# Performance work log

Measured on AMD Instinct MI355X. Metric: run time of the kernel, lower is better.

Reference implementation:

```python
import jax, jax.numpy as jnp
import numpy as np

D_MODEL = 1024
D_HIDDEN = 4096
NUM_BANKS = 16
NUM_SELECTED = 2


def setup_inputs() -> dict:
    key = jax.random.key(0)
    ks = jax.random.split(key, 7)
    s = 0.02
    return {
        "tensor": jax.random.normal(ks[0], (4, 1024, D_MODEL), dtype=jnp.float32),
        "Wr": jax.random.normal(ks[1], (D_MODEL, NUM_BANKS), dtype=jnp.float32) * s,
        "br": jnp.zeros((NUM_BANKS,), dtype=jnp.float32),
        "W1": jax.random.normal(ks[2], (NUM_BANKS, D_MODEL, D_HIDDEN), dtype=jnp.float32) * s,
        "b1": jnp.zeros((NUM_BANKS, D_HIDDEN), dtype=jnp.float32),
        "W2": jax.random.normal(ks[3], (NUM_BANKS, D_HIDDEN, D_MODEL), dtype=jnp.float32) * s,
        "b2": jnp.zeros((NUM_BANKS, D_MODEL), dtype=jnp.float32),
    }


def reference(tensor, Wr, br, W1, b1, W2, b2):
    # Router: softmax over banks, keep top-k probabilities (BankSelector)
    logits = jnp.einsum("bsd,de->bse", tensor, Wr) + br          # [B,S,E]
    probs = jax.nn.softmax(logits, axis=-1)
    topv, topi = jax.lax.top_k(probs, NUM_SELECTED)              # [B,S,K]
    # Dense gate [B,S,E]: selected banks carry their router probability,
    # all other banks are zeroed (equivalent to sparse dispatch/combine).
    gate = jnp.sum(jax.nn.one_hot(topi, NUM_BANKS, dtype=tensor.dtype)
                   * topv[..., None], axis=-2)                    # [B,S,E]
    # Banked expert FFN (BankedLinear x2 with ReLU between)
    h = jax.nn.relu(jnp.einsum("bsd,edh->bseh", tensor, W1) + b1)  # [B,S,E,Dh]
    y = jnp.einsum("bseh,ehm->bsem", h, W2) + b2                   # [B,S,E,Dm]
    # Weighted combine across selected banks
    out = jnp.einsum("bse,bsem->bsm", gate, y)                     # [B,S,Dm]
    return out
```

## Files before the change

kernel.cpp:

```cpp
#include <hip/hip_runtime.h>
#include <stdint.h>

#define D_MODEL   1024
#define D_HIDDEN  4096
#define NBANKS    16
#define NTOK      4096

#define BM 128
#define BN 128
#define BK 32
#define LDSK 56

typedef __attribute__((ext_vector_type(8))) short bf16x8;
typedef __attribute__((ext_vector_type(4))) float f32x4;

__device__ __forceinline__ unsigned short f2bf(float f) {
  unsigned u = __builtin_bit_cast(unsigned, f);
  u += 0x7FFFu + ((u >> 16) & 1u);
  return (unsigned short)(u >> 16);
}

__global__ __launch_bounds__(256) void zero_out_k(float4* __restrict__ out4,
                                                  int* __restrict__ counts) {
  size_t i = (size_t)blockIdx.x * 256 + threadIdx.x;
  out4[i] = make_float4(0.f, 0.f, 0.f, 0.f);
  if (blockIdx.x == 0 && threadIdx.x < NBANKS) counts[threadIdx.x] = 0;
}

__global__ __launch_bounds__(64) void router_k(const float* __restrict__ x,
                                               const float* __restrict__ Wr,
                                               const float* __restrict__ br,
                                               int* __restrict__ topIdx,
                                               float* __restrict__ topGate) {
  const int t = blockIdx.x;
  const int l = threadIdx.x;
  const float* xr = x + (size_t)t * D_MODEL;

  float acc[NBANKS];
#pragma unroll
  for (int e = 0; e < NBANKS; ++e) acc[e] = 0.f;

  for (int d = l; d < D_MODEL; d += 64) {
    const float xv = xr[d];
    const float* wrow = Wr + (size_t)d * NBANKS;
#pragma unroll
    for (int e = 0; e < NBANKS; ++e) acc[e] += xv * wrow[e];
  }
#pragma unroll
  for (int e = 0; e < NBANKS; ++e) {
#pragma unroll
    for (int m = 1; m < 64; m <<= 1) acc[e] += __shfl_xor(acc[e], m, 64);
  }
#pragma unroll
  for (int e = 0; e < NBANKS; ++e) acc[e] += br[e];

  if (l == 0) {
    float mx = acc[0];
#pragma unroll
    for (int e = 1; e < NBANKS; ++e) mx = fmaxf(mx, acc[e]);
    float p[NBANKS];
    float s = 0.f;
#pragma unroll
    for (int e = 0; e < NBANKS; ++e) { p[e] = expf(acc[e] - mx); s += p[e]; }
    int i0 = 0; float v0 = p[0];
#pragma unroll
    for (int e = 1; e < NBANKS; ++e) if (p[e] > v0) { v0 = p[e]; i0 = e; }
    int i1 = -1; float v1 = -1.f;
#pragma unroll
    for (int e = 0; e < NBANKS; ++e) if (e != i0 && p[e] > v1) { v1 = p[e]; i1 = e; }
    const float inv = 1.f / s;
    topIdx[2 * t]     = i0;
    topIdx[2 * t + 1] = i1;
    topGate[2 * t]     = v0 * inv;
    topGate[2 * t + 1] = v1 * inv;
  }
}

__global__ __launch_bounds__(256) void build_lists_k(const int* __restrict__ topIdx,
                                                     const float* __restrict__ topGate,
                                                     int* __restrict__ counts,
                                                     int* __restrict__ rowlist,
                                                     float* __restrict__ gatelist) {
  const int t = blockIdx.x * 256 + threadIdx.x;
  if (t >= NTOK) return;
#pragma unroll
  for (int k = 0; k < 2; ++k) {
    const int e = topIdx[2 * t + k];
    const int p = atomicAdd(&counts[e], 1);
    rowlist[e * NTOK + p]  = t;
    gatelist[e * NTOK + p] = topGate[2 * t + k];
  }
}

__global__ void scan_k(const int* __restrict__ counts, int* __restrict__ bankOff) {
  if (threadIdx.x == 0) {
    int s = 0;
#pragma unroll
    for (int e = 0; e < NBANKS; ++e) { bankOff[e] = s; s += counts[e]; }
    bankOff[NBANKS] = s;
  }
}

__global__ __launch_bounds__(256) void gemm1_k(const float* __restrict__ X,
                                               const float* __restrict__ W1,
                                               const float* __restrict__ b1,
                                               const int* __restrict__ counts,
                                               const int* __restrict__ bankOff,
                                               const int* __restrict__ rowlist,
                                               unsigned short* __restrict__ H) {
  const int e   = blockIdx.z;
  const int cnt = counts[e];
  const int m0  = blockIdx.y * BM;
  if (m0 >= cnt) return;
  const int n0  = blockIdx.x * BN;

  const int tid  = threadIdx.x;
  const int lane = tid & 63;
  const int w    = tid >> 6;
  const int wm   = (w >> 1) * 64;
  const int wn   = (w & 1) * 64;

  __shared__ unsigned short Xs[BM][LDSK];
  __shared__ unsigned short Ws[BN][LDSK];

  const int ar = tid >> 1;
  const int ak = (tid & 1) * 16;
  const int gi = min(m0 + ar, cnt - 1);
  const int tok = rowlist[e * NTOK + gi];
  const float* Arow = X + (size_t)tok * D_MODEL;

  const int bn = tid & 127;
  const int bg = tid >> 7;
  const float* Wb = W1 + (size_t)e * D_MODEL * D_HIDDEN;

  f32x4 acc[4][4];
#pragma unroll
  for (int i = 0; i < 4; ++i)
#pragma unroll
    for (int j = 0; j < 4; ++j)
#pragma unroll
      for (int r = 0; r < 4; ++r) acc[i][j][r] = 0.f;

  for (int k0 = 0; k0 < D_MODEL; k0 += BK) {
    {
      const float4* src = (const float4*)(Arow + k0 + ak);
      const float4 f0 = src[0], f1 = src[1], f2 = src[2], f3 = src[3];
      bf16x8 v0, v1;
      v0[0]=(short)f2bf(f0.x); v0[1]=(short)f2bf(f0.y); v0[2]=(short)f2bf(f0.z); v0[3]=(short)f2bf(f0.w);
      v0[4]=(short)f2bf(f1.x); v0[5]=(short)f2bf(f1.y); v0[6]=(short)f2bf(f1.z); v0[7]=(short)f2bf(f1.w);
      v1[0]=(short)f2bf(f2.x); v1[1]=(short)f2bf(f2.y); v1[2]=(short)f2bf(f2.z); v1[3]=(short)f2bf(f2.w);
      v1[4]=(short)f2bf(f3.x); v1[5]=(short)f2bf(f3.y); v1[6]=(short)f2bf(f3.z); v1[7]=(short)f2bf(f3.w);
      *((bf16x8*)&Xs[ar][ak])     = v0;
      *((bf16x8*)&Xs[ar][ak + 8]) = v1;
    }
#pragma unroll
    for (int i = 0; i < 4; ++i) {
      const int kb = bg * 4 + i * 8;
      const float* wp = Wb + (size_t)(k0 + kb) * D_HIDDEN + n0 + bn;
      const float a0 = wp[0];
      const float a1 = wp[D_HIDDEN];
      const float a2 = wp[2 * D_HIDDEN];
      const float a3 = wp[3 * D_HIDDEN];
      const unsigned long long pv =
          (unsigned long long)f2bf(a0)
        | ((unsigned long long)f2bf(a1) << 16)
        | ((unsigned long long)f2bf(a2) << 32)
        | ((unsigned long long)f2bf(a3) << 48);
      *((unsigned long long*)&Ws[bn][kb]) = pv;
    }
    __syncthreads();

    const int fr = lane & 15;
    const int fc = (lane >> 4) * 8;
    bf16x8 af[4], bfv[4];
#pragma unroll
    for (int mb = 0; mb < 4; ++mb) af[mb]  = *(const bf16x8*)&Xs[wm + mb * 16 + fr][fc];
#pragma unroll
    for (int nb = 0; nb < 4; ++nb) bfv[nb] = *(const bf16x8*)&Ws[wn + nb * 16 + fr][fc];
#pragma unroll
    for (int mb = 0; mb < 4; ++mb)
#pragma unroll
      for (int nb = 0; nb < 4; ++nb)
        acc[mb][nb] = __builtin_amdgcn_mfma_f32_16x16x32_bf16(af[mb], bfv[nb], acc[mb][nb], 0, 0, 0);
    __syncthreads();
  }

  const int hb = bankOff[e] + m0;
#pragma unroll
  for (int nb = 0; nb < 4; ++nb) {
    const int col = n0 + wn + nb * 16 + (lane & 15);
    const float bias = b1[e * D_HIDDEN + col];
#pragma unroll
    for (int mb = 0; mb < 4; ++mb)
#pragma unroll
      for (int r = 0; r < 4; ++r) {
        const int rowT = wm + mb * 16 + (lane >> 4) * 4 + r;
        if (m0 + rowT < cnt) {
          float v = acc[mb][nb][r] + bias;
          v = fmaxf(v, 0.f);
          H[(size_t)(hb + rowT) * D_HIDDEN + col] = f2bf(v);
        }
      }
  }
}

__global__ __launch_bounds__(256) void gemm2_k(const unsigned short* __restrict__ H,
                                               const float* __restrict__ W2,
                                               const float* __restrict__ b2,
                                               const int* __restrict__ counts,
                                               const int* __restrict__ bankOff,
                                               const int* __restrict__ rowlist,
                                               const float* __restrict__ gatelist,
                                               float* __restrict__ out) {
  const int e   = blockIdx.z;
  const int cnt = counts[e];
  const int m0  = blockIdx.y * BM;
  if (m0 >= cnt) return;
  const int n0  = blockIdx.x * BN;

  const int tid  = threadIdx.x;
  const int lane = tid & 63;
  const int w    = tid >> 6;
  const int wm   = (w >> 1) * 64;
  const int wn   = (w & 1) * 64;

  __shared__ unsigned short Xs[BM][LDSK];
  __shared__ unsigned short Ws[BN][LDSK];

  const int ar = tid >> 1;
  const int ak = (tid & 1) * 16;
  const int hb = bankOff[e];
  const int gi = hb + min(m0 + ar, cnt - 1);
  const unsigned short* Arow = H + (size_t)gi * D_HIDDEN;

  const int bn = tid & 127;
  const int bg = tid >> 7;
  const float* Wb = W2 + (size_t)e * D_HIDDEN * D_MODEL;

  f32x4 acc[4][4];
#pragma unroll
  for (int i = 0; i < 4; ++i)
#pragma unroll
    for (int j = 0; j < 4; ++j)
#pragma unroll
      for (int r = 0; r < 4; ++r) acc[i][j][r] = 0.f;

  for (int k0 = 0; k0 < D_HIDDEN; k0 += BK) {
    *((bf16x8*)&Xs[ar][ak])     = *(const bf16x8*)(Arow + k0 + ak);
    *((bf16x8*)&Xs[ar][ak + 8]) = *(const bf16x8*)(Arow + k0 + ak + 8);
#pragma unroll
    for (int i = 0; i < 4; ++i) {
      const int kb = bg * 4 + i * 8;
      const float* wp = Wb + (size_t)(k0 + kb) * D_MODEL + n0 + bn;
      const float a0 = wp[0];
      const float a1 = wp[D_MODEL];
      const float a2 = wp[2 * D_MODEL];
      const float a3 = wp[3 * D_MODEL];
      const unsigned long long pv =
          (unsigned long long)f2bf(a0)
        | ((unsigned long long)f2bf(a1) << 16)
        | ((unsigned long long)f2bf(a2) << 32)
        | ((unsigned long long)f2bf(a3) << 48);
      *((unsigned long long*)&Ws[bn][kb]) = pv;
    }
    __syncthreads();

    const int fr = lane & 15;
    const int fc = (lane >> 4) * 8;
    bf16x8 af[4], bfv[4];
#pragma unroll
    for (int mb = 0; mb < 4; ++mb) af[mb]  = *(const bf16x8*)&Xs[wm + mb * 16 + fr][fc];
#pragma unroll
    for (int nb = 0; nb < 4; ++nb) bfv[nb] = *(const bf16x8*)&Ws[wn + nb * 16 + fr][fc];
#pragma unroll
    for (int mb = 0; mb < 4; ++mb)
#pragma unroll
      for (int nb = 0; nb < 4; ++nb)
        acc[mb][nb] = __builtin_amdgcn_mfma_f32_16x16x32_bf16(af[mb], bfv[nb], acc[mb][nb], 0, 0, 0);
    __syncthreads();
  }

  float bias[4];
#pragma unroll
  for (int nb = 0; nb < 4; ++nb)
    bias[nb] = b2[e * D_MODEL + n0 + wn + nb * 16 + (lane & 15)];

#pragma unroll
  for (int mb = 0; mb < 4; ++mb)
#pragma unroll
    for (int r = 0; r < 4; ++r) {
      const int rowT = wm + mb * 16 + (lane >> 4) * 4 + r;
      if (m0 + rowT < cnt) {
        const int sidx = e * NTOK + m0 + rowT;
        const int tok  = rowlist[sidx];
        const float g  = gatelist[sidx];
        float* orow = out + (size_t)tok * D_MODEL;
#pragma unroll
        for (int nb = 0; nb < 4; ++nb) {
          const int col = n0 + wn + nb * 16 + (lane & 15);
          atomicAdd(&orow[col], g * (acc[mb][nb][r] + bias[nb]));
        }
      }
    }
}

extern "C" void kernel_launch(void* const* d_in, const int* in_sizes, int n_in,
                              void* d_out, int out_size, void* d_ws, size_t ws_size,
                              hipStream_t stream) {
  const float* X  = (const float*)d_in[0];
  const float* Wr = (const float*)d_in[1];
  const float* br = (const float*)d_in[2];
  const float* W1 = (const float*)d_in[3];
  const float* b1 = (const float*)d_in[4];
  const float* W2 = (const float*)d_in[5];
  const float* b2 = (const float*)d_in[6];
  float* out = (float*)d_out;

  char* w = (char*)d_ws;
  int*   topIdx   = (int*)(w);
  float* topGate  = (float*)(w + (32 << 10));
  int*   counts   = (int*)(w + (64 << 10));
  int*   bankOff  = (int*)(w + (64 << 10) + 256);
  int*   rowlist  = (int*)(w + (66 << 10));
  float* gatelist = (float*)(w + (66 << 10) + NBANKS * NTOK * 4);
  unsigned short* H = (unsigned short*)(w + (1 << 20));

  const size_t needed = (size_t)(1 << 20) + (size_t)(NTOK * 2) * D_HIDDEN * 2;
  if (ws_size < needed) return;

  zero_out_k<<<dim3(4096), dim3(256), 0, stream>>>((float4*)out, counts);
  router_k<<<dim3(NTOK), dim3(64), 0, stream>>>(X, Wr, br, topIdx, topGate);
  build_lists_k<<<dim3(16), dim3(256), 0, stream>>>(topIdx, topGate, counts, rowlist, gatelist);
  scan_k<<<dim3(1), dim3(64), 0, stream>>>(counts, bankOff);
  gemm1_k<<<dim3(D_HIDDEN / BN, NTOK / BM, NBANKS), dim3(256), 0, stream>>>(
      X, W1, b1, counts, bankOff, rowlist, H);
  gemm2_k<<<dim3(D_MODEL / BN, NTOK / BM, NBANKS), dim3(256), 0, stream>>>(
      H, W2, b2, counts, bankOff, rowlist, gatelist, out);
}
```

Measured before the change: 498.9 us.

## Swizzle LDS tiles, vectorize weight loads and use packed bf16 conversion

Replaces padded LDS arrays with an XOR-swizzled unpadded layout to avoid bank conflicts. Weight tile loads become float4 reads covering a 4x4 block per thread, transposed in registers, instead of scalar strided loads. FP32-to-bf16 conversion uses the packed v_cvt_pk_bf16_f32 instruction instead of manual rounding. LDS fragment addresses are precomputed outside the K loop. This reduces global load instruction count and ALU conversion overhead, but the swizzle pattern must avoid new conflicts on the 8-byte weight stores.

```diff
diff --git a/kernel.cpp b/kernel.cpp
--- a/kernel.cpp
+++ b/kernel.cpp
@@ -9,15 +9,27 @@
 #define BM 128
 #define BN 128
 #define BK 32
-#define LDSK 56
 
 typedef __attribute__((ext_vector_type(8))) short bf16x8;
 typedef __attribute__((ext_vector_type(4))) float f32x4;
+typedef __attribute__((ext_vector_type(4))) unsigned int u32x4;
+typedef __attribute__((ext_vector_type(2))) unsigned int u32x2;
 
 __device__ __forceinline__ unsigned short f2bf(float f) {
   unsigned u = __builtin_bit_cast(unsigned, f);
   u += 0x7FFFu + ((u >> 16) & 1u);
   return (unsigned short)(u >> 16);
+}
+
+__device__ __forceinline__ unsigned cvtpk(float lo, float hi) {
+  unsigned r;
+  asm("v_cvt_pk_bf16_f32 %0, %1, %2" : "=v"(r) : "v"(lo), "v"(hi));
+  return r;
+}
+
+__device__ __forceinline__ int swz(int row, int col) {
+  const int c = (col >> 3) ^ ((row >> 1) & 3);
+  return row * 32 + c * 8 + (col & 7);
 }
 
 __global__ __launch_bounds__(256) void zero_out_k(float4* __restrict__ out4,
@@ -120,18 +132,34 @@
   const int wm   = (w >> 1) * 64;
   const int wn   = (w & 1) * 64;
 
-  __shared__ unsigned short Xs[BM][LDSK];
-  __shared__ unsigned short Ws[BN][LDSK];
+  __shared__ unsigned short Xs[BM * BK];
+  __shared__ unsigned short Ws[BN * BK];
 
   const int ar = tid >> 1;
   const int ak = (tid & 1) * 16;
   const int gi = min(m0 + ar, cnt - 1);
   const int tok = rowlist[e * NTOK + gi];
-  const float* Arow = X + (size_t)tok * D_MODEL;
-
-  const int bn = tid & 127;
-  const int bg = tid >> 7;
-  const float* Wb = W1 + (size_t)e * D_MODEL * D_HIDDEN;
+  const float* Asrc = X + (size_t)tok * D_MODEL + ak;
+  unsigned short* xsw0 = &Xs[swz(ar, ak)];
+  unsigned short* xsw1 = &Xs[swz(ar, ak + 8)];
+
+  const int bn4 = (tid & 31) * 4;
+  const int bk4 = (tid >> 5) * 4;
+  const float* Bsrc = W1 + (size_t)e * D_MODEL * D_HIDDEN + (size_t)bk4 * D_HIDDEN + n0 + bn4;
+  unsigned short* wsw0 = &Ws[swz(bn4 + 0, bk4)];
+  unsigned short* wsw1 = &Ws[swz(bn4 + 1, bk4)];
+  unsigned short* wsw2 = &Ws[swz(bn4 + 2, bk4)];
+  unsigned short* wsw3 = &Ws[swz(bn4 + 3, bk4)];
+
+  const int fr = lane & 15;
+  const int fc = (lane >> 4) * 8;
+  const unsigned short* arp[4];
+  const unsigned short* brp[4];
+#pragma unroll
+  for (int i = 0; i < 4; ++i) {
+    arp[i] = &Xs[swz(wm + i * 16 + fr, fc)];
+    brp[i] = &Ws[swz(wn + i * 16 + fr, fc)];
+  }
 
   f32x4 acc[4][4];
 #pragma unroll
@@ -143,40 +171,39 @@
 
   for (int k0 = 0; k0 < D_MODEL; k0 += BK) {
     {
-      const float4* src = (const float4*)(Arow + k0 + ak);
-      const float4 f0 = src[0], f1 = src[1], f2 = src[2], f3 = src[3];
-      bf16x8 v0, v1;
-      v0[0]=(short)f2bf(f0.x); v0[1]=(short)f2bf(f0.y); v0[2]=(short)f2bf(f0.z); v0[3]=(short)f2bf(f0.w);
-      v0[4]=(short)f2bf(f1.x); v0[5]=(short)f2bf(f1.y); v0[6]=(short)f2bf(f1.z); v0[7]=(short)f2bf(f1.w);
-      v1[0]=(short)f2bf(f2.x); v1[1]=(short)f2bf(f2.y); v1[2]=(short)f2bf(f2.z); v1[3]=(short)f2bf(f2.w);
-      v1[4]=(short)f2bf(f3.x); v1[5]=(short)f2bf(f3.y); v1[6]=(short)f2bf(f3.z); v1[7]=(short)f2bf(f3.w);
-      *((bf16x8*)&Xs[ar][ak])     = v0;
-      *((bf16x8*)&Xs[ar][ak + 8]) = v1;
+      const float4* s4 = (const float4*)(Asrc + k0);
+      const float4 f0 = s4[0], f1 = s4[1], f2 = s4[2], f3 = s4[3];
+      u32x4 v0, v1;
+      v0[0] = cvtpk(f0.x, f0.y); v0[1] = cvtpk(f0.z, f0.w);
+      v0[2] = cvtpk(f1.x, f1.y); v0[3] = cvtpk(f1.z, f1.w);
+      v1[0] = cvtpk(f2.x, f2.y); v1[1] = cvtpk(f2.z, f2.w);
+      v1[2] = cvtpk(f3.x, f3.y); v1[3] = cvtpk(f3.z, f3.w);
+      *((u32x4*)xsw0) = v0;
+      *((u32x4*)xsw1) = v1;
     }
-#pragma unroll
-    for (int i = 0; i < 4; ++i) {
-      const int kb = bg * 4 + i * 8;
-      const float* wp = Wb + (size_t)(k0 + kb) * D_HIDDEN + n0 + bn;
-      const float a0 = wp[0];
-      const float a1 = wp[D_HIDDEN];
-      const float a2 = wp[2 * D_HIDDEN];
-      const float a3 = wp[3 * D_HIDDEN];
-      const unsigned long long pv =
-          (unsigned long long)f2bf(a0)
-        | ((unsigned long long)f2bf(a1) << 16)
-        | ((unsigned long long)f2bf(a2) << 32)
-        | ((unsigned long long)f2bf(a3) << 48);
-      *((unsigned long long*)&Ws[bn][kb]) = pv;
+    {
+      const float* wp = Bsrc + (size_t)k0 * D_HIDDEN;
+      const float4 r0 = *(const float4*)(wp);
+      const float4 r1 = *(const float4*)(wp + D_HIDDEN);
+      const float4 r2 = *(const float4*)(wp + 2 * D_HIDDEN);
+      const float4 r3 = *(const float4*)(wp + 3 * D_HIDDEN);
+      u32x2 t0, t1, t2, t3;
+      t0[0] = cvtpk(r0.x, r1.x); t0[1] = cvtpk(r2.x, r3.x);
+      t1[0] = cvtpk(r0.y, r1.y); t1[1] = cvtpk(r2.y, r3.y);
+      t2[0] = cvtpk(r0.z, r1.z); t2[1] = cvtpk(r2.z, r3.z);
+      t3[0] = cvtpk(r0.w, r1.w); t3[1] = cvtpk(r2.w, r3.w);
+      *((u32x2*)wsw0) = t0;
+      *((u32x2*)wsw1) = t1;
+      *((u32x2*)wsw2) = t2;
+      *((u32x2*)wsw3) = t3;
     }
     __syncthreads();
 
-    const int fr = lane & 15;
-    const int fc = (lane >> 4) * 8;
     bf16x8 af[4], bfv[4];
 #pragma unroll
-    for (int mb = 0; mb < 4; ++mb) af[mb]  = *(const bf16x8*)&Xs[wm + mb * 16 + fr][fc];
-#pragma unroll
-    for (int nb = 0; nb < 4; ++nb) bfv[nb] = *(const bf16x8*)&Ws[wn + nb * 16 + fr][fc];
+    for (int mb = 0; mb < 4; ++mb) af[mb]  = *(const bf16x8*)arp[mb];
+#pragma unroll
+    for (int nb = 0; nb < 4; ++nb) bfv[nb] = *(const bf16x8*)brp[nb];
 #pragma unroll
     for (int mb = 0; mb < 4; ++mb)
 #pragma unroll
@@ -224,18 +251,34 @@
   const int wm   = (w >> 1) * 64;
   const int wn   = (w & 1) * 64;
 
-  __shared__ unsigned short Xs[BM][LDSK];
-  __shared__ unsigned short Ws[BN][LDSK];
+  __shared__ unsigned short Xs[BM * BK];
+  __shared__ unsigned short Ws[BN * BK];
 
   const int ar = tid >> 1;
   const int ak = (tid & 1) * 16;
   const int hb = bankOff[e];
   const int gi = hb + min(m0 + ar, cnt - 1);
-  const unsigned short* Arow = H + (size_t)gi * D_HIDDEN;
-
-  const int bn = tid & 127;
-  const int bg = tid >> 7;
-  const float* Wb = W2 + (size_t)e * D_HIDDEN * D_MODEL;
+  const unsigned short* Asrc = H + (size_t)gi * D_HIDDEN + ak;
+  unsigned short* xsw0 = &Xs[swz(ar, ak)];
+  unsigned short* xsw1 = &Xs[swz(ar, ak + 8)];
+
+  const int bn4 = (tid & 31) * 4;
+  const int bk4 = (tid >> 5) * 4;
+  const float* Bsrc = W2 + (size_t)e * D_HIDDEN * D_MODEL + (size_t)bk4 * D_MODEL + n0 + bn4;
+  unsigned short* wsw0 = &Ws[swz(bn4 + 0, bk4)];
+  unsigned short* wsw1 = &Ws[swz(bn4 + 1, bk4)];
+  unsigned short* wsw2 = &Ws[swz(bn4 + 2, bk4)];
+  unsigned short* wsw3 = &Ws[swz(bn4 + 3, bk4)];
+
+  const int fr = lane & 15;
+  const int fc = (lane >> 4) * 8;
+  const unsigned short* arp[4];
+  const unsigned short* brp[4];
+#pragma unroll
+  for (int i = 0; i < 4; ++i) {
+    arp[i] = &Xs[swz(wm + i * 16 + fr, fc)];
+    brp[i] = &Ws[swz(wn + i * 16 + fr, fc)];
+  }
 
   f32x4 acc[4][4];
 #pragma unroll
@@ -246,32 +289,31 @@
       for (int r = 0; r < 4; ++r) acc[i][j][r] = 0.f;
 
   for (int k0 = 0; k0 < D_HIDDEN; k0 += BK) {
-    *((bf16x8*)&Xs[ar][ak])     = *(const bf16x8*)(Arow + k0 + ak);
-    *((bf16x8*)&Xs[ar][ak + 8]) = *(const bf16x8*)(Arow + k0 + ak + 8);
-#pragma unroll
-    for (int i = 0; i < 4; ++i) {
-      const int kb = bg * 4 + i * 8;
-      const float* wp = Wb + (size_t)(k0 + kb) * D_MODEL + n0 + bn;
-      const float a0 = wp[0];
-      const float a1 = wp[D_MODEL];
-      const float a2 = wp[2 * D_MODEL];
-      const float a3 = wp[3 * D_MODEL];
-      const unsigned long long pv =
-          (unsigned long long)f2bf(a0)
-        | ((unsigned long long)f2bf(a1) << 16)
-        | ((unsigned long long)f2bf(a2) << 32)
-        | ((unsigned long long)f2bf(a3) << 48);
-      *((unsigned long long*)&Ws[bn][kb]) = pv;
+    *((bf16x8*)xsw0) = *(const bf16x8*)(Asrc + k0);
+    *((bf16x8*)xsw1) = *(const bf16x8*)(Asrc + k0 + 8);
+    {
+      const float* wp = Bsrc + (size_t)k0 * D_MODEL;
+      const float4 r0 = *(const float4*)(wp);
+      const float4 r1 = *(const float4*)(wp + D_MODEL);
+      const float4 r2 = *(const float4*)(wp + 2 * D_MODEL);
+      const float4 r3 = *(const float4*)(wp + 3 * D_MODEL);
+      u32x2 t0, t1, t2, t3;
+      t0[0] = cvtpk(r0.x, r1.x); t0[1] = cvtpk(r2.x, r3.x);
+      t1[0] = cvtpk(r0.y, r1.y); t1[1] = cvtpk(r2.y, r3.y);
+      t2[0] = cvtpk(r0.z, r1.z); t2[1] = cvtpk(r2.z, r3.z);
+      t3[0] = cvtpk(r0.w, r1.w); t3[1] = cvtpk(r2.w, r3.w);
+      *((u32x2*)wsw0) = t0;
+      *((u32x2*)wsw1) = t1;
+      *((u32x2*)wsw2) = t2;
+      *((u32x2*)wsw3) = t3;
     }
     __syncthreads();
 
-    const int fr = lane & 15;
-    const int fc = (lane >> 4) * 8;
     bf16x8 af[4], bfv[4];
 #pragma unroll
-    for (int mb = 0; mb < 4; ++mb) af[mb]  = *(const bf16x8*)&Xs[wm + mb * 16 + fr][fc];
-#pragma unroll
-    for (int nb = 0; nb < 4; ++nb) bfv[nb] = *(const bf16x8*)&Ws[wn + nb * 16 + fr][fc];
+    for (int mb = 0; mb < 4; ++mb) af[mb]  = *(const bf16x8*)arp[mb];
+#pragma unroll
+    for (int nb = 0; nb < 4; ++nb) bfv[nb] = *(const bf16x8*)brp[nb];
 #pragma unroll
     for (int mb = 0; mb < 4; ++mb)
 #pragma unroll
```

Result: no change. 496.0 us (-0.6%).

## Double-buffer global loads via registers, widen K tile, swizzle LDS, packed bf16 convert

Applied to the files above, without the earlier changes.

Both expert GEMMs now prefetch the next K tile from global memory into registers while computing on the current LDS tile. BK grows from 32 to 64 and the padded LDS layout is replaced by an XOR swizzle. Weight loads become float4 vectors converted with the packed v_cvt_pk_bf16_f32 instruction, and launch bounds request 2 blocks per CU. This is meant to hide global load latency and cut conversion and instruction overhead, at the cost of more registers and an extra barrier per iteration.

```diff
diff --git a/kernel.cpp b/kernel.cpp
--- a/kernel.cpp
+++ b/kernel.cpp
@@ -8,16 +8,26 @@
 
 #define BM 128
 #define BN 128
-#define BK 32
-#define LDSK 56
+#define BK 64
 
 typedef __attribute__((ext_vector_type(8))) short bf16x8;
 typedef __attribute__((ext_vector_type(4))) float f32x4;
+typedef __attribute__((ext_vector_type(4))) unsigned int u32x4;
 
 __device__ __forceinline__ unsigned short f2bf(float f) {
   unsigned u = __builtin_bit_cast(unsigned, f);
   u += 0x7FFFu + ((u >> 16) & 1u);
   return (unsigned short)(u >> 16);
+}
+
+__device__ __forceinline__ unsigned cvtpk(float lo, float hi) {
+  unsigned r;
+  asm("v_cvt_pk_bf16_f32 %0, %1, %2" : "=v"(r) : "v"(lo), "v"(hi));
+  return r;
+}
+
+__device__ __forceinline__ int sidx(int r, int k) {
+  return (r << 6) + ((((k >> 3) ^ (r & 7)) << 3) | (k & 7));
 }
 
 __global__ __launch_bounds__(256) void zero_out_k(float4* __restrict__ out4,
@@ -101,13 +111,13 @@
   }
 }
 
-__global__ __launch_bounds__(256) void gemm1_k(const float* __restrict__ X,
-                                               const float* __restrict__ W1,
-                                               const float* __restrict__ b1,
-                                               const int* __restrict__ counts,
-                                               const int* __restrict__ bankOff,
-                                               const int* __restrict__ rowlist,
-                                               unsigned short* __restrict__ H) {
+__global__ __launch_bounds__(256, 2) void gemm1_k(const float* __restrict__ X,
+                                                  const float* __restrict__ W1,
+                                                  const float* __restrict__ b1,
+                                                  const int* __restrict__ counts,
+                                                  const int* __restrict__ bankOff,
+                                                  const int* __restrict__ rowlist,
+                                                  unsigned short* __restrict__ H) {
   const int e   = blockIdx.z;
   const int cnt = counts[e];
   const int m0  = blockIdx.y * BM;
@@ -120,18 +130,30 @@
   const int wm   = (w >> 1) * 64;
   const int wn   = (w & 1) * 64;
 
-  __shared__ unsigned short Xs[BM][LDSK];
-  __shared__ unsigned short Ws[BN][LDSK];
-
-  const int ar = tid >> 1;
-  const int ak = (tid & 1) * 16;
-  const int gi = min(m0 + ar, cnt - 1);
-  const int tok = rowlist[e * NTOK + gi];
-  const float* Arow = X + (size_t)tok * D_MODEL;
-
-  const int bn = tid & 127;
-  const int bg = tid >> 7;
-  const float* Wb = W1 + (size_t)e * D_MODEL * D_HIDDEN;
+  __shared__ unsigned short Xs[BM * BK];
+  __shared__ unsigned short Ws[BN * BK];
+
+  const int arow = tid >> 1;
+  const int akh  = (tid & 1) * 32;
+  const int gi   = min(m0 + arow, cnt - 1);
+  const int tok  = rowlist[e * NTOK + gi];
+  const float* Asrc = X + (size_t)tok * D_MODEL + akh;
+  unsigned short* xw[4];
+#pragma unroll
+  for (int j = 0; j < 4; ++j) xw[j] = &Xs[sidx(arow, akh + 8 * j)];
+
+  const int nrb = 4 * (tid & 7) + 32 * (tid >> 6);
+  const int kb  = 8 * ((tid >> 3) & 7);
+  const float* Bsrc = W1 + (size_t)e * D_MODEL * D_HIDDEN + (size_t)kb * D_HIDDEN + n0 + nrb;
+  unsigned short* ww[4];
+#pragma unroll
+  for (int i = 0; i < 4; ++i) ww[i] = &Ws[sidx(nrb + i, kb)];
+
+  const int fr = lane & 15;
+  const int fc = (lane >> 4) * 8;
+
+  float raf[8][4];
+  float rbf[8][4];
 
   f32x4 acc[4][4];
 #pragma unroll
@@ -141,60 +163,79 @@
 #pragma unroll
       for (int r = 0; r < 4; ++r) acc[i][j][r] = 0.f;
 
-  for (int k0 = 0; k0 < D_MODEL; k0 += BK) {
-    {
-      const float4* src = (const float4*)(Arow + k0 + ak);
-      const float4 f0 = src[0], f1 = src[1], f2 = src[2], f3 = src[3];
-      bf16x8 v0, v1;
-      v0[0]=(short)f2bf(f0.x); v0[1]=(short)f2bf(f0.y); v0[2]=(short)f2bf(f0.z); v0[3]=(short)f2bf(f0.w);
-      v0[4]=(short)f2bf(f1.x); v0[5]=(short)f2bf(f1.y); v0[6]=(short)f2bf(f1.z); v0[7]=(short)f2bf(f1.w);
-      v1[0]=(short)f2bf(f2.x); v1[1]=(short)f2bf(f2.y); v1[2]=(short)f2bf(f2.z); v1[3]=(short)f2bf(f2.w);
-      v1[4]=(short)f2bf(f3.x); v1[5]=(short)f2bf(f3.y); v1[6]=(short)f2bf(f3.z); v1[7]=(short)f2bf(f3.w);
-      *((bf16x8*)&Xs[ar][ak])     = v0;
-      *((bf16x8*)&Xs[ar][ak + 8]) = v1;
+  auto LOAD = [&](int t) {
+    const float* ap = Asrc + t * BK;
+#pragma unroll
+    for (int j = 0; j < 8; ++j)
+      *(float4*)&raf[j][0] = *(const float4*)(ap + 4 * j);
+    const float* bp = Bsrc + (size_t)t * BK * D_HIDDEN;
+#pragma unroll
+    for (int kk = 0; kk < 8; ++kk)
+      *(float4*)&rbf[kk][0] = *(const float4*)(bp + (size_t)kk * D_HIDDEN);
+  };
+
+  auto WRITE = [&]() {
+#pragma unroll
+    for (int j = 0; j < 4; ++j) {
+      u32x4 v;
+      v[0] = cvtpk(raf[2*j][0], raf[2*j][1]);
+      v[1] = cvtpk(raf[2*j][2], raf[2*j][3]);
+      v[2] = cvtpk(raf[2*j+1][0], raf[2*j+1][1]);
+      v[3] = cvtpk(raf[2*j+1][2], raf[2*j+1][3]);
+      *(u32x4*)xw[j] = v;
     }
 #pragma unroll
     for (int i = 0; i < 4; ++i) {
-      const int kb = bg * 4 + i * 8;
-      const float* wp = Wb + (size_t)(k0 + kb) * D_HIDDEN + n0 + bn;
-      const float a0 = wp[0];
-      const float a1 = wp[D_HIDDEN];
-      const float a2 = wp[2 * D_HIDDEN];
-      const float a3 = wp[3 * D_HIDDEN];
-      const unsigned long long pv =
-          (unsigned long long)f2bf(a0)
-        | ((unsigned long long)f2bf(a1) << 16)
-        | ((unsigned long long)f2bf(a2) << 32)
-        | ((unsigned long long)f2bf(a3) << 48);
-      *((unsigned long long*)&Ws[bn][kb]) = pv;
-    }
+      u32x4 v;
+      v[0] = cvtpk(rbf[0][i], rbf[1][i]);
+      v[1] = cvtpk(rbf[2][i], rbf[3][i]);
+      v[2] = cvtpk(rbf[4][i], rbf[5][i]);
+      v[3] = cvtpk(rbf[6][i], rbf[7][i]);
+      *(u32x4*)ww[i] = v;
+    }
+  };
+
+  auto COMPUTE = [&]() {
+#pragma unroll
+    for (int h = 0; h < 2; ++h) {
+      bf16x8 af[4], bb[4];
+#pragma unroll
+      for (int mb = 0; mb < 4; ++mb)
+        af[mb] = *(const bf16x8*)&Xs[sidx(wm + mb * 16 + fr, h * 32 + fc)];
+#pragma unroll
+      for (int nb = 0; nb < 4; ++nb)
+        bb[nb] = *(const bf16x8*)&Ws[sidx(wn + nb * 16 + fr, h * 32 + fc)];
+#pragma unroll
+      for (int mb = 0; mb < 4; ++mb)
+#pragma unroll
+        for (int nb = 0; nb < 4; ++nb)
+          acc[mb][nb] = __builtin_amdgcn_mfma_f32_16x16x32_bf16(af[mb], bb[nb], acc[mb][nb], 0, 0, 0);
+    }
+  };
+
+  const int NT = D_MODEL / BK;
+  LOAD(0);
+  WRITE();
+  __syncthreads();
+#pragma unroll 1
+  for (int t = 0; t < NT; ++t) {
+    if (t + 1 < NT) LOAD(t + 1);
+    COMPUTE();
     __syncthreads();
-
-    const int fr = lane & 15;
-    const int fc = (lane >> 4) * 8;
-    bf16x8 af[4], bfv[4];
-#pragma unroll
-    for (int mb = 0; mb < 4; ++mb) af[mb]  = *(const bf16x8*)&Xs[wm + mb * 16 + fr][fc];
-#pragma unroll
-    for (int nb = 0; nb < 4; ++nb) bfv[nb] = *(const bf16x8*)&Ws[wn + nb * 16 + fr][fc];
+    if (t + 1 < NT) { WRITE(); __syncthreads(); }
+  }
+
+  const int hb = bankOff[e] + m0;
+  const int rq = (lane >> 4) * 4;
+#pragma unroll
+  for (int nb = 0; nb < 4; ++nb) {
+    const int col = n0 + wn + nb * 16 + fr;
+    const float bias = b1[e * D_HIDDEN + col];
 #pragma unroll
     for (int mb = 0; mb < 4; ++mb)
 #pragma unroll
-      for (int nb = 0; nb < 4; ++nb)
-        acc[mb][nb] = __builtin_amdgcn_mfma_f32_16x16x32_bf16(af[mb], bfv[nb], acc[mb][nb], 0, 0, 0);
-    __syncthreads();
-  }
-
-  const int hb = bankOff[e] + m0;
-#pragma unroll
-  for (int nb = 0; nb < 4; ++nb) {
-    const int col = n0 + wn + nb * 16 + (lane & 15);
-    const float bias = b1[e * D_HIDDEN + col];
-#pragma unroll
-    for (int mb = 0; mb < 4; ++mb)
-#pragma unroll
       for (int r = 0; r < 4; ++r) {
-        const int rowT = wm + mb * 16 + (lane >> 4) * 4 + r;
+        const int rowT = wm + mb * 16 + rq + r;
         if (m0 + rowT < cnt) {
           float v = acc[mb][nb][r] + bias;
           v = fmaxf(v, 0.f);
@@ -204,14 +245,14 @@
   }
 }
 
-__global__ __launch_bounds__(256) void gemm2_k(const unsigned short* __restrict__ H,
-                                               const float* __restrict__ W2,
-                                               const float* __restrict__ b2,
-                                               const int* __restrict__ counts,
-                                               const int* __restrict__ bankOff,
-                                               const int* __restrict__ rowlist,
-                                               const float* __restrict__ gatelist,
-                                               float* __restrict__ out) {
+__global__ __launch_bounds__(256, 2) void gemm2_k(const unsigned short* __restrict__ H,
+                                                  const float* __restrict__ W2,
+                                                  const float* __restrict__ b2,
+                                                  const int* __restrict__ counts,
+                                                  const int* __restrict__ bankOff,
+                                                  const int* __restrict__ rowlist,
+                                                  const float* __restrict__ gatelist,
+                                                  float* __restrict__ out) {
   const int e   = blockIdx.z;
   const int cnt = counts[e];
   const int m0  = blockIdx.y * BM;
@@ -224,18 +265,30 @@
   const int wm   = (w >> 1) * 64;
   const int wn   = (w & 1) * 64;
 
-  __shared__ unsigned short Xs[BM][LDSK];
-  __shared__ unsigned short Ws[BN][LDSK];
-
-  const int ar = tid >> 1;
-  const int ak = (tid & 1) * 16;
-  const int hb = bankOff[e];
-  const int gi = hb + min(m0 + ar, cnt - 1);
-  const unsigned short* Arow = H + (size_t)gi * D_HIDDEN;
-
-  const int bn = tid & 127;
-  const int bg = tid >> 7;
-  const float* Wb = W2 + (size_t)e * D_HIDDEN * D_MODEL;
+  __shared__ unsigned short Xs[BM * BK];
+  __shared__ unsigned short Ws[BN * BK];
+
+  const int arow = tid >> 1;
+  const int akh  = (tid & 1) * 32;
+  const int hb   = bankOff[e];
+  const int gi   = hb + min(m0 + arow, cnt - 1);
+  const unsigned short* Asrc = H + (size_t)gi * D_HIDDEN + akh;
+  unsigned short* xw[4];
+#pragma unroll
+  for (int j = 0; j < 4; ++j) xw[j] = &Xs[sidx(arow, akh + 8 * j)];
+
+  const int nrb = 4 * (tid & 7) + 32 * (tid >> 6);
+  const int kb  = 8 * ((tid >> 3) & 7);
+  const float* Bsrc = W2 + (size_t)e * D_HIDDEN * D_MODEL + (size_t)kb * D_MODEL + n0 + nrb;
+  unsigned short* ww[4];
+#pragma unroll
+  for (int i = 0; i < 4; ++i) ww[i] = &Ws[sidx(nrb + i, kb)];
+
+  const int fr = lane & 15;
+  const int fc = (lane >> 4) * 8;
+
+  bf16x8 ha[4];
+  float rbf[8][4];
 
   f32x4 acc[4][4];
 #pragma unroll
@@ -245,59 +298,79 @@
 #pragma unroll
       for (int r = 0; r < 4; ++r) acc[i][j][r] = 0.f;
 
-  for (int k0 = 0; k0 < D_HIDDEN; k0 += BK) {
-    *((bf16x8*)&Xs[ar][ak])     = *(const bf16x8*)(Arow + k0 + ak);
-    *((bf16x8*)&Xs[ar][ak + 8]) = *(const bf16x8*)(Arow + k0 + ak + 8);
+  auto LOAD = [&](int t) {
+    const unsigned short* ap = Asrc + t * BK;
+#pragma unroll
+    for (int j = 0; j < 4; ++j) ha[j] = *(const bf16x8*)(ap + 8 * j);
+    const float* bp = Bsrc + (size_t)t * BK * D_MODEL;
+#pragma unroll
+    for (int kk = 0; kk < 8; ++kk)
+      *(float4*)&rbf[kk][0] = *(const float4*)(bp + (size_t)kk * D_MODEL);
+  };
+
+  auto WRITE = [&]() {
+#pragma unroll
+    for (int j = 0; j < 4; ++j) *(bf16x8*)xw[j] = ha[j];
 #pragma unroll
     for (int i = 0; i < 4; ++i) {
-      const int kb = bg * 4 + i * 8;
-      const float* wp = Wb + (size_t)(k0 + kb) * D_MODEL + n0 + bn;
-      const float a0 = wp[0];
-      const float a1 = wp[D_MODEL];
-      const float a2 = wp[2 * D_MODEL];
-      const float a3 = wp[3 * D_MODEL];
-      const unsigned long long pv =
-          (unsigned long long)f2bf(a0)
-        | ((unsigned long long)f2bf(a1) << 16)
-        | ((unsigned long long)f2bf(a2) << 32)
-        | ((unsigned long long)f2bf(a3) << 48);
-      *((unsigned long long*)&Ws[bn][kb]) = pv;
-    }
+      u32x4 v;
+      v[0] = cvtpk(rbf[0][i], rbf[1][i]);
+      v[1] = cvtpk(rbf[2][i], rbf[3][i]);
+      v[2] = cvtpk(rbf[4][i], rbf[5][i]);
+      v[3] = cvtpk(rbf[6][i], rbf[7][i]);
+      *(u32x4*)ww[i] = v;
+    }
+  };
+
+  auto COMPUTE = [&]() {
+#pragma unroll
+    for (int h = 0; h < 2; ++h) {
+      bf16x8 af[4], bb[4];
+#pragma unroll
+      for (int mb = 0; mb < 4; ++mb)
+        af[mb] = *(const bf16x8*)&Xs[sidx(wm + mb * 16 + fr, h * 32 + fc)];
+#pragma unroll
+      for (int nb = 0; nb < 4; ++nb)
+        bb[nb] = *(const bf16x8*)&Ws[sidx(wn + nb * 16 + fr, h * 32 + fc)];
+#pragma unroll
+      for (int mb = 0; mb < 4; ++mb)
+#pragma unroll
+        for (int nb = 0; nb < 4; ++nb)
+          acc[mb][nb] = __builtin_amdgcn_mfma_f32_16x16x32_bf16(af[mb], bb[nb], acc[mb][nb], 0, 0, 0);
+    }
+  };
+
+  const int NT = D_HIDDEN / BK;
+  LOAD(0);
+  WRITE();
+  __syncthreads();
+#pragma unroll 1
+  for (int t = 0; t < NT; ++t) {
+    if (t + 1 < NT) LOAD(t + 1);
+    COMPUTE();
     __syncthreads();
-
-    const int fr = lane & 15;
-    const int fc = (lane >> 4) * 8;
-    bf16x8 af[4], bfv[4];
-#pragma unroll
-    for (int mb = 0; mb < 4; ++mb) af[mb]  = *(const bf16x8*)&Xs[wm + mb * 16 + fr][fc];
-#pragma unroll
-    for (int nb = 0; nb < 4; ++nb) bfv[nb] = *(const bf16x8*)&Ws[wn + nb * 16 + fr][fc];
-#pragma unroll
-    for (int mb = 0; mb < 4; ++mb)
-#pragma unroll
-      for (int nb = 0; nb < 4; ++nb)
-        acc[mb][nb] = __builtin_amdgcn_mfma_f32_16x16x32_bf16(af[mb], bfv[nb], acc[mb][nb], 0, 0, 0);
-    __syncthreads();
-  }
-
+    if (t + 1 < NT) { WRITE(); __syncthreads(); }
+  }
+
+  const int rq = (lane >> 4) * 4;
   float bias[4];
 #pragma unroll
   for (int nb = 0; nb < 4; ++nb)
-    bias[nb] = b2[e * D_MODEL + n0 + wn + nb * 16 + (lane & 15)];
+    bias[nb] = b2[e * D_MODEL + n0 + wn + nb * 16 + fr];
 
 #pragma unroll
   for (int mb = 0; mb < 4; ++mb)
 #pragma unroll
     for (int r = 0; r < 4; ++r) {
-      const int rowT = wm + mb * 16 + (lane >> 4) * 4 + r;
+      const int rowT = wm + mb * 16 + rq + r;
       if (m0 + rowT < cnt) {
-        const int sidx = e * NTOK + m0 + rowT;
-        const int tok  = rowlist[sidx];
-        const float g  = gatelist[sidx];
+        const int sidx2 = e * NTOK + m0 + rowT;
+        const int tok   = rowlist[sidx2];
+        const float g   = gatelist[sidx2];
         float* orow = out + (size_t)tok * D_MODEL;
 #pragma unroll
         for (int nb = 0; nb < 4; ++nb) {
-          const int col = n0 + wn + nb * 16 + (lane & 15);
+          const int col = n0 + wn + nb * 16 + fr;
           atomicAdd(&orow[col], g * (acc[mb][nb][r] + bias[nb]));
         }
       }
```

Result: slower. 535.6 us (+7.4%).
